# Kernel tuning notes

Measured on AMD Instinct MI355X. Metric: run time of the kernel, lower is better.

Reference implementation:

```python
import math
import jax, jax.numpy as jnp
import numpy as np

N, L, H, E, K = 4, 768, 8, 64, 1  # batch, seq (L==S), heads, feat, num_sines


def setup_inputs() -> dict:
    key = jax.random.key(0)
    ks = jax.random.split(key, 8)
    queries = jax.random.normal(ks[0], (N, L, H, E), jnp.float32)
    keys = jax.random.normal(ks[1], (N, L, H, E), jnp.float32)
    values = jax.random.normal(ks[2], (N, L, H, E), jnp.float32)
    attn_mask_add = jnp.zeros((L, L), jnp.float32)
    key_lengths_add = jnp.zeros((N, L), jnp.float32)
    freqs = jax.random.normal(ks[3], (H, E, K), jnp.float32) - 4.0  # init shift
    offsets = jax.random.normal(ks[4], (H, E, K), jnp.float32)
    gains = jax.random.normal(ks[5], (H, E, K), jnp.float32)
    # gains.data /= sqrt(||gains||_{-1}) / 2
    gains = gains / (jnp.sqrt(jnp.linalg.norm(gains, axis=-1, keepdims=True)) / 2.0)
    gate = jax.random.normal(ks[6], (H, E), jnp.float32)
    return dict(queries=queries, keys=keys, values=values,
                attn_mask_add=attn_mask_add, key_lengths_add=key_lengths_add,
                freqs=freqs, offsets=offsets, gains=gains, gate=gate)


def reference(queries, keys, values, attn_mask_add, key_lengths_add,
              freqs, offsets, gains, gate):
    n, l, h, e = queries.shape
    softmax_temp = 1.0 / math.sqrt(e)
    positions = jnp.arange(l, dtype=queries.dtype)  # (L,)
    f = jax.nn.sigmoid(freqs)[None] / 2.0  # (1,H,E,K)
    phases_q = 2.0 * math.pi * f * positions[:, None, None, None] + offsets[None]
    phases_k = 2.0 * math.pi * f * positions[:, None, None, None]
    # interleave cos/sin along last dim -> (L,H,E,2K)
    omega_q = jnp.stack([jnp.cos(phases_q), jnp.sin(phases_q)], axis=-1).reshape(l, h, e, 2 * f.shape[-1])
    omega_k = jnp.stack([jnp.cos(phases_k), jnp.sin(phases_k)], axis=-1).reshape(l, h, e, 2 * f.shape[-1])
    g = jax.nn.softplus(gains)
    g2 = jnp.stack([g, g], axis=-1).reshape(h, e, 2 * f.shape[-1])  # (H,E,2K)
    # positional kernel P: (L,S,H,E)
    P = jnp.einsum('lhdk,hdk,shdk->lshd', omega_q, g2 ** 2, omega_k)
    P = (1.0 - gate) * P + gate  # gated
    QK = jnp.einsum('nlhd,lshd,nshd->nhls', queries, P, keys)
    QK = QK + attn_mask_add[None, None] + key_lengths_add[:, None, None, :]
    A = jax.nn.softmax(softmax_temp * QK, axis=-1)
    V = jnp.einsum('nhls,nshd->nlhd', A, values)
    return V
```

## Files before the change

kernel.cpp:

```cpp
#include <hip/hip_runtime.h>
#include <math.h>
#include <stdint.h>

#define NB 4
#define LQ 768
#define NH 8
#define NE 64
#define ND 192
#define TEMP 0.125f

typedef _Float16 f16;
typedef __attribute__((ext_vector_type(8))) _Float16 f16x8;
typedef __attribute__((ext_vector_type(4))) float f32x4;

__device__ __forceinline__ void stage16(f16* lds_base, const f16* g, int lane) {
#if __has_builtin(__builtin_amdgcn_global_load_lds)
    __builtin_amdgcn_global_load_lds(
        (const __attribute__((address_space(1))) uint32_t*)g,
        (__attribute__((address_space(3))) uint32_t*)lds_base, 16, 0, 0);
#else
    *(uint4*)((char*)lds_base + lane * 16) = *(const uint4*)g;
#endif
}

__global__ __launch_bounds__(256) void sinattn_prep(
    const float* __restrict__ Q, const float* __restrict__ K,
    const float* __restrict__ freqs, const float* __restrict__ offsets,
    const float* __restrict__ gains, const float* __restrict__ gate,
    f16* __restrict__ Qf, f16* __restrict__ Kf)
{
    int idx = blockIdx.x * 256 + threadIdx.x;
    int eg = idx & 7, e0 = eg << 3;
    int h  = (idx >> 3) & 7;
    int t  = idx >> 6;
    int l  = t % LQ;
    int n  = t / LQ;
    int nh = (n << 3) | h;
    int he = (h << 6) | e0;

    const float* qp = Q + (size_t)idx * 8;
    const float* kp = K + (size_t)idx * 8;
    float4 q0 = *(const float4*)qp, q1 = *(const float4*)(qp + 4);
    float4 k0 = *(const float4*)kp, k1 = *(const float4*)(kp + 4);
    float qv[8] = {q0.x,q0.y,q0.z,q0.w, q1.x,q1.y,q1.z,q1.w};
    float kv[8] = {k0.x,k0.y,k0.z,k0.w, k1.x,k1.y,k1.z,k1.w};

    float4 fA = *(const float4*)(freqs   + he), fB = *(const float4*)(freqs   + he + 4);
    float4 oA = *(const float4*)(offsets + he), oB = *(const float4*)(offsets + he + 4);
    float4 gA = *(const float4*)(gains   + he), gB = *(const float4*)(gains   + he + 4);
    float4 tA = *(const float4*)(gate    + he), tB = *(const float4*)(gate    + he + 4);
    float fv[8] = {fA.x,fA.y,fA.z,fA.w, fB.x,fB.y,fB.z,fB.w};
    float ov[8] = {oA.x,oA.y,oA.z,oA.w, oB.x,oB.y,oB.z,oB.w};
    float gv[8] = {gA.x,gA.y,gA.z,gA.w, gB.x,gB.y,gB.z,gB.w};
    float tv[8] = {tA.x,tA.y,tA.z,tA.w, tB.x,tB.y,tB.z,tB.w};

    f16x8 oq0, oq1, oq2, ok0, ok1, ok2;
    float lf = (float)l;
    #pragma unroll
    for (int j = 0; j < 8; ++j) {
        float f  = 0.5f / (1.0f + __expf(-fv[j]));
        float gn = gv[j];
        float sp = (gn > 15.0f) ? gn : __logf(1.0f + __expf(gn));
        float gt = tv[j];
        float a  = (1.0f - gt) * sp * sp;
        float fh = __uint_as_float(__float_as_uint(f) & 0xFFFFF000u);
        float fl = f - fh;
        float t0 = lf * fh;
        float tr = t0 - floorf(t0);
        tr = __builtin_fmaf(lf, fl, tr);
        float pk = 6.28318530717958647f * tr;
        float pq = pk + ov[j];
        float sq = __sinf(pq), cq = __cosf(pq);
        float sk = __sinf(pk), ck = __cosf(pk);
        oq0[j] = (f16)(qv[j] * a * cq);
        oq1[j] = (f16)(qv[j] * a * sq);
        oq2[j] = (f16)(qv[j] * gt);
        ok0[j] = (f16)(kv[j] * ck);
        ok1[j] = (f16)(kv[j] * sk);
        ok2[j] = (f16)(kv[j]);
    }
    size_t base = ((size_t)nh * LQ + l) * ND + e0;
    *(f16x8*)(Qf + base)            = oq0;
    *(f16x8*)(Qf + base + NE)       = oq1;
    *(f16x8*)(Qf + base + 2 * NE)   = oq2;
    *(f16x8*)(Kf + base)            = ok0;
    *(f16x8*)(Kf + base + NE)       = ok1;
    *(f16x8*)(Kf + base + 2 * NE)   = ok2;
}

__global__ __launch_bounds__(256) void sinattn_vt(
    const float* __restrict__ V, f16* __restrict__ Vt)
{
    __shared__ f16 tile[64][72];
    int b = blockIdx.x;
    int st = b % 12, nh = b / 12;
    int n = nh >> 3, h = nh & 7;
    int s0 = st * 64;
    int tid = threadIdx.x;

    int sl = tid >> 2, e0 = (tid & 3) << 4;
    const float4* vp = (const float4*)(V + ((size_t)(n * LQ + s0 + sl) * NH + h) * NE + e0);
    float4 a0 = vp[0], a1 = vp[1], a2 = vp[2], a3 = vp[3];
    float vv[16] = { a0.x,a0.y,a0.z,a0.w, a1.x,a1.y,a1.z,a1.w,
                     a2.x,a2.y,a2.z,a2.w, a3.x,a3.y,a3.z,a3.w };
    #pragma unroll
    for (int j = 0; j < 16; ++j) tile[e0 + j][sl] = (f16)vv[j];
    __syncthreads();

    int er = tid >> 2, sc = tid & 3;
    f16* op = Vt + ((size_t)nh * NE + er) * LQ + s0 + sc * 16;
    *(uint4*)op       = *(const uint4*)&tile[er][sc * 16];
    *(uint4*)(op + 8) = *(const uint4*)&tile[er][sc * 16 + 8];
}

__global__ __launch_bounds__(256, 2) void sinattn_flash(
    const f16* __restrict__ Qf, const f16* __restrict__ Kf, const f16* __restrict__ Vt,
    const float* __restrict__ mask, const float* __restrict__ keylen,
    float* __restrict__ out)
{
    __shared__ __attribute__((aligned(16))) f16 sK[2][64 * 24 * 8];
    __shared__ __attribute__((aligned(16))) f16 sV[2][64 * 8 * 8];
    __shared__ __attribute__((aligned(16))) f16 sP[4][16 * 72];

    int tid  = threadIdx.x;
    int wv   = tid >> 6;
    int lane = tid & 63;
    int grp  = lane >> 4;
    int r16  = lane & 15;
    int swz  = r16 & 7;

    int bid = blockIdx.x;
    int nh  = bid & 31;
    int lt  = bid >> 5;
    int n   = nh >> 3;
    int l0  = lt * 64;

    f16x8 qf[6];
    {
        size_t rbase = ((size_t)nh * LQ + l0 + wv * 16 + r16) * ND + grp * 8;
        #pragma unroll
        for (int d0 = 0; d0 < 6; ++d0)
            qf[d0] = *(const f16x8*)(Qf + rbase + d0 * 32);
    }

    int goffK[6], goffV[2];
    #pragma unroll
    for (int i = 0; i < 6; ++i) {
        int p = i * 256 + wv * 64 + lane;
        int r = p / 24, c = p - r * 24;
        int cl = (c & ~7) | ((c & 7) ^ (r & 7));
        goffK[i] = r * ND + cl * 8;
    }
    #pragma unroll
    for (int i = 0; i < 2; ++i) {
        int p = i * 256 + wv * 64 + lane;
        int r = p >> 3, c = p & 7;
        goffV[i] = r * LQ + (c ^ (r & 7)) * 8;
    }
    const f16* Kb = Kf + (size_t)nh * LQ * ND;
    const f16* Vb = Vt + (size_t)nh * NE * LQ;

    {
        #pragma unroll
        for (int i = 0; i < 6; ++i)
            stage16(&sK[0][(i * 256 + wv * 64) * 8], Kb + goffK[i], lane);
        #pragma unroll
        for (int i = 0; i < 2; ++i)
            stage16(&sV[0][(i * 256 + wv * 64) * 8], Vb + goffV[i], lane);
    }

    float m_i[4], l_i[4];
    f32x4 O[4];
    #pragma unroll
    for (int rr = 0; rr < 4; ++rr) { m_i[rr] = -INFINITY; l_i[rr] = 0.f; }
    #pragma unroll
    for (int tt = 0; tt < 4; ++tt)
        #pragma unroll
        for (int rr = 0; rr < 4; ++rr) O[tt][rr] = 0.f;

    for (int c = 0; c < 12; ++c) {
        int cur = c & 1;
        int s0  = c * 64;
        __syncthreads();

        if (c < 11) {
            const f16* kg = Kb + (s0 + 64) * ND;
            const f16* vg = Vb + (s0 + 64);
            #pragma unroll
            for (int i = 0; i < 6; ++i)
                stage16(&sK[cur ^ 1][(i * 256 + wv * 64) * 8], kg + goffK[i], lane);
            #pragma unroll
            for (int i = 0; i < 2; ++i)
                stage16(&sV[cur ^ 1][(i * 256 + wv * 64) * 8], vg + goffV[i], lane);
        }

        float klv[4], mreg[4][4];
        #pragma unroll
        for (int j = 0; j < 4; ++j) klv[j] = keylen[n * LQ + s0 + j * 16 + r16];
        #pragma unroll
        for (int rr = 0; rr < 4; ++rr) {
            int lrow = l0 + wv * 16 + grp * 4 + rr;
            #pragma unroll
            for (int j = 0; j < 4; ++j)
                mreg[rr][j] = mask[lrow * LQ + s0 + j * 16 + r16];
        }

        f32x4 st[4];
        #pragma unroll
        for (int j = 0; j < 4; ++j)
            #pragma unroll
            for (int rr = 0; rr < 4; ++rr) st[j][rr] = 0.f;
        #pragma unroll
        for (int d0 = 0; d0 < 6; ++d0) {
            #pragma unroll
            for (int j = 0; j < 4; ++j) {
                int cc = d0 * 4 + grp;
                int cl = (cc & ~7) | ((cc & 7) ^ swz);
                f16x8 bf = *(const f16x8*)&sK[cur][((j * 16 + r16) * 24 + cl) * 8];
                st[j] = __builtin_amdgcn_mfma_f32_16x16x32_f16(qf[d0], bf, st[j], 0, 0, 0);
            }
        }

        #pragma unroll
        for (int rr = 0; rr < 4; ++rr) {
            float lg[4];
            float mx = -INFINITY;
            #pragma unroll
            for (int j = 0; j < 4; ++j) {
                lg[j] = TEMP * (st[j][rr] + mreg[rr][j] + klv[j]);
                mx = fmaxf(mx, lg[j]);
            }
            #pragma unroll
            for (int d = 1; d < 16; d <<= 1) mx = fmaxf(mx, __shfl_xor(mx, d));
            float mnew  = fmaxf(m_i[rr], mx);
            float alpha = __expf(m_i[rr] - mnew);
            float rs = 0.f;
            #pragma unroll
            for (int j = 0; j < 4; ++j) {
                float p = __expf(lg[j] - mnew);
                rs += p;
                sP[wv][(grp * 4 + rr) * 72 + j * 16 + r16] = (f16)p;
            }
            #pragma unroll
            for (int d = 1; d < 16; d <<= 1) rs += __shfl_xor(rs, d);
            l_i[rr] = l_i[rr] * alpha + rs;
            m_i[rr] = mnew;
            #pragma unroll
            for (int tt = 0; tt < 4; ++tt) O[tt][rr] *= alpha;
        }

        #pragma unroll
        for (int kk = 0; kk < 2; ++kk) {
            f16x8 pa = *(const f16x8*)&sP[wv][r16 * 72 + kk * 32 + grp * 8];
            #pragma unroll
            for (int tt = 0; tt < 4; ++tt) {
                int cc = kk * 4 + grp;
                f16x8 vb = *(const f16x8*)&sV[cur][((tt * 16 + r16) * 8 + (cc ^ swz)) * 8];
                O[tt] = __builtin_amdgcn_mfma_f32_16x16x32_f16(pa, vb, O[tt], 0, 0, 0);
            }
        }
    }

    #pragma unroll
    for (int rr = 0; rr < 4; ++rr) {
        float inv = 1.0f / l_i[rr];
        int lrow = l0 + wv * 16 + grp * 4 + rr;
        float* op = out + ((size_t)(n * LQ + lrow) * NH + (nh & 7)) * NE;
        #pragma unroll
        for (int tt = 0; tt < 4; ++tt)
            op[tt * 16 + r16] = O[tt][rr] * inv;
    }
}

extern "C" void kernel_launch(void* const* d_in, const int* in_sizes, int n_in,
                              void* d_out, int out_size, void* d_ws, size_t ws_size,
                              hipStream_t stream)
{
    const float* Q      = (const float*)d_in[0];
    const float* K      = (const float*)d_in[1];
    const float* V      = (const float*)d_in[2];
    const float* mask   = (const float*)d_in[3];
    const float* keylen = (const float*)d_in[4];
    const float* freqs  = (const float*)d_in[5];
    const float* offs   = (const float*)d_in[6];
    const float* gains  = (const float*)d_in[7];
    const float* gate   = (const float*)d_in[8];
    float* out = (float*)d_out;

    const size_t P = (size_t)NB * NH * LQ * ND;
    f16* Qf = (f16*)d_ws;
    f16* Kf = Qf + P;
    f16* Vt = Kf + P;

    sinattn_prep<<<768, 256, 0, stream>>>(Q, K, freqs, offs, gains, gate, Qf, Kf);
    sinattn_vt<<<384, 256, 0, stream>>>(V, Vt);
    sinattn_flash<<<NB * NH * (LQ / 64), 256, 0, stream>>>(Qf, Kf, Vt,
                                                           mask, keylen, out);
}
```

Baseline: 121.6 us.

## Load K and V MFMA operands directly from global memory instead of LDS

Removes the double-buffered LDS staging of K and V tiles and the per-chunk block barrier. Each wave now reads its MFMA B operands straight from global memory, relying on L2/L1 to serve the data shared among the four waves of a block. It also raises wave priority around the MFMA sections with s_setprio. The risk is redundant global traffic, since each wave now fetches the full K/V chunk separately, and exposed load latency with no explicit prefetch.

New measurement: 183.7 us. +51.1%, slower.

```diff
diff --git a/kernel.cpp b/kernel.cpp
--- a/kernel.cpp
+++ b/kernel.cpp
@@ -12,16 +12,6 @@
 typedef _Float16 f16;
 typedef __attribute__((ext_vector_type(8))) _Float16 f16x8;
 typedef __attribute__((ext_vector_type(4))) float f32x4;
-
-__device__ __forceinline__ void stage16(f16* lds_base, const f16* g, int lane) {
-#if __has_builtin(__builtin_amdgcn_global_load_lds)
-    __builtin_amdgcn_global_load_lds(
-        (const __attribute__((address_space(1))) uint32_t*)g,
-        (__attribute__((address_space(3))) uint32_t*)lds_base, 16, 0, 0);
-#else
-    *(uint4*)((char*)lds_base + lane * 16) = *(const uint4*)g;
-#endif
-}
 
 __global__ __launch_bounds__(256) void sinattn_prep(
     const float* __restrict__ Q, const float* __restrict__ K,
@@ -118,8 +108,6 @@
     const float* __restrict__ mask, const float* __restrict__ keylen,
     float* __restrict__ out)
 {
-    __shared__ __attribute__((aligned(16))) f16 sK[2][64 * 24 * 8];
-    __shared__ __attribute__((aligned(16))) f16 sV[2][64 * 8 * 8];
     __shared__ __attribute__((aligned(16))) f16 sP[4][16 * 72];
 
     int tid  = threadIdx.x;
@@ -127,7 +115,6 @@
     int lane = tid & 63;
     int grp  = lane >> 4;
     int r16  = lane & 15;
-    int swz  = r16 & 7;
 
     int bid = blockIdx.x;
     int nh  = bid & 31;
@@ -143,31 +130,8 @@
             qf[d0] = *(const f16x8*)(Qf + rbase + d0 * 32);
     }
 
-    int goffK[6], goffV[2];
-    #pragma unroll
-    for (int i = 0; i < 6; ++i) {
-        int p = i * 256 + wv * 64 + lane;
-        int r = p / 24, c = p - r * 24;
-        int cl = (c & ~7) | ((c & 7) ^ (r & 7));
-        goffK[i] = r * ND + cl * 8;
-    }
-    #pragma unroll
-    for (int i = 0; i < 2; ++i) {
-        int p = i * 256 + wv * 64 + lane;
-        int r = p >> 3, c = p & 7;
-        goffV[i] = r * LQ + (c ^ (r & 7)) * 8;
-    }
-    const f16* Kb = Kf + (size_t)nh * LQ * ND;
-    const f16* Vb = Vt + (size_t)nh * NE * LQ;
-
-    {
-        #pragma unroll
-        for (int i = 0; i < 6; ++i)
-            stage16(&sK[0][(i * 256 + wv * 64) * 8], Kb + goffK[i], lane);
-        #pragma unroll
-        for (int i = 0; i < 2; ++i)
-            stage16(&sV[0][(i * 256 + wv * 64) * 8], Vb + goffV[i], lane);
-    }
+    const f16* Kb = Kf + (size_t)nh * LQ * ND + (size_t)r16 * ND + grp * 8;
+    const f16* Vb = Vt + ((size_t)nh * NE + r16) * LQ + grp * 8;
 
     float m_i[4], l_i[4];
     f32x4 O[4];
@@ -179,20 +143,7 @@
         for (int rr = 0; rr < 4; ++rr) O[tt][rr] = 0.f;
 
     for (int c = 0; c < 12; ++c) {
-        int cur = c & 1;
-        int s0  = c * 64;
-        __syncthreads();
-
-        if (c < 11) {
-            const f16* kg = Kb + (s0 + 64) * ND;
-            const f16* vg = Vb + (s0 + 64);
-            #pragma unroll
-            for (int i = 0; i < 6; ++i)
-                stage16(&sK[cur ^ 1][(i * 256 + wv * 64) * 8], kg + goffK[i], lane);
-            #pragma unroll
-            for (int i = 0; i < 2; ++i)
-                stage16(&sV[cur ^ 1][(i * 256 + wv * 64) * 8], vg + goffV[i], lane);
-        }
+        int s0 = c * 64;
 
         float klv[4], mreg[4][4];
         #pragma unroll
@@ -210,16 +161,16 @@
         for (int j = 0; j < 4; ++j)
             #pragma unroll
             for (int rr = 0; rr < 4; ++rr) st[j][rr] = 0.f;
+        __builtin_amdgcn_s_setprio(1);
         #pragma unroll
         for (int d0 = 0; d0 < 6; ++d0) {
             #pragma unroll
             for (int j = 0; j < 4; ++j) {
-                int cc = d0 * 4 + grp;
-                int cl = (cc & ~7) | ((cc & 7) ^ swz);
-                f16x8 bf = *(const f16x8*)&sK[cur][((j * 16 + r16) * 24 + cl) * 8];
+                f16x8 bf = *(const f16x8*)(Kb + (size_t)(s0 + j * 16) * ND + d0 * 32);
                 st[j] = __builtin_amdgcn_mfma_f32_16x16x32_f16(qf[d0], bf, st[j], 0, 0, 0);
             }
         }
+        __builtin_amdgcn_s_setprio(0);
 
         #pragma unroll
         for (int rr = 0; rr < 4; ++rr) {
@@ -249,16 +200,17 @@
             for (int tt = 0; tt < 4; ++tt) O[tt][rr] *= alpha;
         }
 
+        __builtin_amdgcn_s_setprio(1);
         #pragma unroll
         for (int kk = 0; kk < 2; ++kk) {
             f16x8 pa = *(const f16x8*)&sP[wv][r16 * 72 + kk * 32 + grp * 8];
             #pragma unroll
             for (int tt = 0; tt < 4; ++tt) {
-                int cc = kk * 4 + grp;
-                f16x8 vb = *(const f16x8*)&sV[cur][((tt * 16 + r16) * 8 + (cc ^ swz)) * 8];
+                f16x8 vb = *(const f16x8*)(Vb + (size_t)(tt * 16) * LQ + s0 + kk * 32);
                 O[tt] = __builtin_amdgcn_mfma_f32_16x16x32_f16(pa, vb, O[tt], 0, 0, 0);
             }
         }
+        __builtin_amdgcn_s_setprio(0);
     }
 
     #pragma unroll
```

## Use two waves per block each computing 32 query rows, DPP row reductions

Applied to the files above, without the earlier changes.

The flash kernel drops from four waves of 16 query rows to two waves of 32 rows, so each K/V fragment read from LDS feeds two MFMAs, halving LDS B-operand traffic per FLOP. Each thread now issues twice as many async global->LDS loads to fill the tiles. Softmax row max/sum reductions switch from __shfl_xor to DPP row operations to avoid LDS-backed shuffles. The cost is more registers per thread and fewer waves per block (128 threads) to hide latency.

Result: no change. 122.4 us (+0.7%).

```diff
diff --git a/kernel.cpp b/kernel.cpp
--- a/kernel.cpp
+++ b/kernel.cpp
@@ -21,6 +21,28 @@
 #else
     *(uint4*)((char*)lds_base + lane * 16) = *(const uint4*)g;
 #endif
+}
+
+template <int CTRL>
+__device__ __forceinline__ float dppf(float x) {
+    union { float f; int i; } u, r;
+    u.f = x;
+    r.i = __builtin_amdgcn_update_dpp(u.i, u.i, CTRL, 0xF, 0xF, false);
+    return r.f;
+}
+__device__ __forceinline__ float red16_max(float x) {
+    x = fmaxf(x, dppf<0xB1>(x));
+    x = fmaxf(x, dppf<0x4E>(x));
+    x = fmaxf(x, dppf<0x141>(x));
+    x = fmaxf(x, dppf<0x140>(x));
+    return x;
+}
+__device__ __forceinline__ float red16_sum(float x) {
+    x += dppf<0xB1>(x);
+    x += dppf<0x4E>(x);
+    x += dppf<0x141>(x);
+    x += dppf<0x140>(x);
+    return x;
 }
 
 __global__ __launch_bounds__(256) void sinattn_prep(
@@ -113,14 +135,14 @@
     *(uint4*)(op + 8) = *(const uint4*)&tile[er][sc * 16 + 8];
 }
 
-__global__ __launch_bounds__(256, 2) void sinattn_flash(
+__global__ __launch_bounds__(128, 2) void sinattn_flash(
     const f16* __restrict__ Qf, const f16* __restrict__ Kf, const f16* __restrict__ Vt,
     const float* __restrict__ mask, const float* __restrict__ keylen,
     float* __restrict__ out)
 {
     __shared__ __attribute__((aligned(16))) f16 sK[2][64 * 24 * 8];
     __shared__ __attribute__((aligned(16))) f16 sV[2][64 * 8 * 8];
-    __shared__ __attribute__((aligned(16))) f16 sP[4][16 * 72];
+    __shared__ __attribute__((aligned(16))) f16 sP[2][32 * 72];
 
     int tid  = threadIdx.x;
     int wv   = tid >> 6;
@@ -135,25 +157,26 @@
     int n   = nh >> 3;
     int l0  = lt * 64;
 
-    f16x8 qf[6];
-    {
-        size_t rbase = ((size_t)nh * LQ + l0 + wv * 16 + r16) * ND + grp * 8;
+    f16x8 qf[2][6];
+    #pragma unroll
+    for (int ti = 0; ti < 2; ++ti) {
+        size_t rbase = ((size_t)nh * LQ + l0 + wv * 32 + ti * 16 + r16) * ND + grp * 8;
         #pragma unroll
         for (int d0 = 0; d0 < 6; ++d0)
-            qf[d0] = *(const f16x8*)(Qf + rbase + d0 * 32);
-    }
-
-    int goffK[6], goffV[2];
-    #pragma unroll
-    for (int i = 0; i < 6; ++i) {
-        int p = i * 256 + wv * 64 + lane;
+            qf[ti][d0] = *(const f16x8*)(Qf + rbase + d0 * 32);
+    }
+
+    int goffK[12], goffV[4];
+    #pragma unroll
+    for (int i = 0; i < 12; ++i) {
+        int p = i * 128 + tid;
         int r = p / 24, c = p - r * 24;
         int cl = (c & ~7) | ((c & 7) ^ (r & 7));
         goffK[i] = r * ND + cl * 8;
     }
     #pragma unroll
-    for (int i = 0; i < 2; ++i) {
-        int p = i * 256 + wv * 64 + lane;
+    for (int i = 0; i < 4; ++i) {
+        int p = i * 128 + tid;
         int r = p >> 3, c = p & 7;
         goffV[i] = r * LQ + (c ^ (r & 7)) * 8;
     }
@@ -162,21 +185,25 @@
 
     {
         #pragma unroll
-        for (int i = 0; i < 6; ++i)
-            stage16(&sK[0][(i * 256 + wv * 64) * 8], Kb + goffK[i], lane);
-        #pragma unroll
-        for (int i = 0; i < 2; ++i)
-            stage16(&sV[0][(i * 256 + wv * 64) * 8], Vb + goffV[i], lane);
-    }
-
-    float m_i[4], l_i[4];
-    f32x4 O[4];
-    #pragma unroll
-    for (int rr = 0; rr < 4; ++rr) { m_i[rr] = -INFINITY; l_i[rr] = 0.f; }
-    #pragma unroll
-    for (int tt = 0; tt < 4; ++tt)
-        #pragma unroll
-        for (int rr = 0; rr < 4; ++rr) O[tt][rr] = 0.f;
+        for (int i = 0; i < 12; ++i)
+            stage16(&sK[0][(i * 128 + wv * 64) * 8], Kb + goffK[i], lane);
+        #pragma unroll
+        for (int i = 0; i < 4; ++i)
+            stage16(&sV[0][(i * 128 + wv * 64) * 8], Vb + goffV[i], lane);
+    }
+
+    float m_i[2][4], l_i[2][4];
+    f32x4 O[2][4];
+    #pragma unroll
+    for (int ti = 0; ti < 2; ++ti)
+        #pragma unroll
+        for (int rr = 0; rr < 4; ++rr) { m_i[ti][rr] = -INFINITY; l_i[ti][rr] = 0.f; }
+    #pragma unroll
+    for (int ti = 0; ti < 2; ++ti)
+        #pragma unroll
+        for (int tt = 0; tt < 4; ++tt)
+            #pragma unroll
+            for (int rr = 0; rr < 4; ++rr) O[ti][tt][rr] = 0.f;
 
     for (int c = 0; c < 12; ++c) {
         int cur = c & 1;
@@ -187,29 +214,33 @@
             const f16* kg = Kb + (s0 + 64) * ND;
             const f16* vg = Vb + (s0 + 64);
             #pragma unroll
-            for (int i = 0; i < 6; ++i)
-                stage16(&sK[cur ^ 1][(i * 256 + wv * 64) * 8], kg + goffK[i], lane);
-            #pragma unroll
-            for (int i = 0; i < 2; ++i)
-                stage16(&sV[cur ^ 1][(i * 256 + wv * 64) * 8], vg + goffV[i], lane);
-        }
-
-        float klv[4], mreg[4][4];
+            for (int i = 0; i < 12; ++i)
+                stage16(&sK[cur ^ 1][(i * 128 + wv * 64) * 8], kg + goffK[i], lane);
+            #pragma unroll
+            for (int i = 0; i < 4; ++i)
+                stage16(&sV[cur ^ 1][(i * 128 + wv * 64) * 8], vg + goffV[i], lane);
+        }
+
+        float klv[4], mreg[2][4][4];
         #pragma unroll
         for (int j = 0; j < 4; ++j) klv[j] = keylen[n * LQ + s0 + j * 16 + r16];
         #pragma unroll
-        for (int rr = 0; rr < 4; ++rr) {
-            int lrow = l0 + wv * 16 + grp * 4 + rr;
+        for (int ti = 0; ti < 2; ++ti)
+            #pragma unroll
+            for (int rr = 0; rr < 4; ++rr) {
+                int lrow = l0 + wv * 32 + ti * 16 + grp * 4 + rr;
+                #pragma unroll
+                for (int j = 0; j < 4; ++j)
+                    mreg[ti][rr][j] = mask[lrow * LQ + s0 + j * 16 + r16];
+            }
+
+        f32x4 st[2][4];
+        #pragma unroll
+        for (int ti = 0; ti < 2; ++ti)
             #pragma unroll
             for (int j = 0; j < 4; ++j)
-                mreg[rr][j] = mask[lrow * LQ + s0 + j * 16 + r16];
-        }
-
-        f32x4 st[4];
-        #pragma unroll
-        for (int j = 0; j < 4; ++j)
-            #pragma unroll
-            for (int rr = 0; rr < 4; ++rr) st[j][rr] = 0.f;
+                #pragma unroll
+                for (int rr = 0; rr < 4; ++rr) st[ti][j][rr] = 0.f;
         #pragma unroll
         for (int d0 = 0; d0 < 6; ++d0) {
             #pragma unroll
@@ -217,58 +248,65 @@
                 int cc = d0 * 4 + grp;
                 int cl = (cc & ~7) | ((cc & 7) ^ swz);
                 f16x8 bf = *(const f16x8*)&sK[cur][((j * 16 + r16) * 24 + cl) * 8];
-                st[j] = __builtin_amdgcn_mfma_f32_16x16x32_f16(qf[d0], bf, st[j], 0, 0, 0);
+                st[0][j] = __builtin_amdgcn_mfma_f32_16x16x32_f16(qf[0][d0], bf, st[0][j], 0, 0, 0);
+                st[1][j] = __builtin_amdgcn_mfma_f32_16x16x32_f16(qf[1][d0], bf, st[1][j], 0, 0, 0);
             }
         }
 
         #pragma unroll
-        for (int rr = 0; rr < 4; ++rr) {
-            float lg[4];
-            float mx = -INFINITY;
-            #pragma unroll
-            for (int j = 0; j < 4; ++j) {
-                lg[j] = TEMP * (st[j][rr] + mreg[rr][j] + klv[j]);
-                mx = fmaxf(mx, lg[j]);
+        for (int ti = 0; ti < 2; ++ti) {
+            #pragma unroll
+            for (int rr = 0; rr < 4; ++rr) {
+                float lg[4];
+                float mx = -INFINITY;
+                #pragma unroll
+                for (int j = 0; j < 4; ++j) {
+                    lg[j] = TEMP * (st[ti][j][rr] + mreg[ti][rr][j] + klv[j]);
+                    mx = fmaxf(mx, lg[j]);
+                }
+                mx = red16_max(mx);
+                float mnew  = fmaxf(m_i[ti][rr], mx);
+                float alpha = __expf(m_i[ti][rr] - mnew);
+                float rs = 0.f;
+                #pragma unroll
+                for (int j = 0; j < 4; ++j) {
+                    float p = __expf(lg[j] - mnew);
+                    rs += p;
+                    sP[wv][(ti * 16 + grp * 4 + rr) * 72 + j * 16 + r16] = (f16)p;
+                }
+                rs = red16_sum(rs);
+                l_i[ti][rr] = l_i[ti][rr] * alpha + rs;
+                m_i[ti][rr] = mnew;
+                #pragma unroll
+                for (int tt = 0; tt < 4; ++tt) O[ti][tt][rr] *= alpha;
             }
-            #pragma unroll
-            for (int d = 1; d < 16; d <<= 1) mx = fmaxf(mx, __shfl_xor(mx, d));
-            float mnew  = fmaxf(m_i[rr], mx);
-            float alpha = __expf(m_i[rr] - mnew);
-            float rs = 0.f;
-            #pragma unroll
-            for (int j = 0; j < 4; ++j) {
-                float p = __expf(lg[j] - mnew);
-                rs += p;
-                sP[wv][(grp * 4 + rr) * 72 + j * 16 + r16] = (f16)p;
-            }
-            #pragma unroll
-            for (int d = 1; d < 16; d <<= 1) rs += __shfl_xor(rs, d);
-            l_i[rr] = l_i[rr] * alpha + rs;
-            m_i[rr] = mnew;
-            #pragma unroll
-            for (int tt = 0; tt < 4; ++tt) O[tt][rr] *= alpha;
         }
 
         #pragma unroll
         for (int kk = 0; kk < 2; ++kk) {
-            f16x8 pa = *(const f16x8*)&sP[wv][r16 * 72 + kk * 32 + grp * 8];
+            f16x8 pa0 = *(const f16x8*)&sP[wv][(r16) * 72 + kk * 32 + grp * 8];
+            f16x8 pa1 = *(const f16x8*)&sP[wv][(16 + r16) * 72 + kk * 32 + grp * 8];
             #pragma unroll
             for (int tt = 0; tt < 4; ++tt) {
                 int cc = kk * 4 + grp;
                 f16x8 vb = *(const f16x8*)&sV[cur][((tt * 16 + r16) * 8 + (cc ^ swz)) * 8];
-                O[tt] = __builtin_amdgcn_mfma_f32_16x16x32_f16(pa, vb, O[tt], 0, 0, 0);
+                O[0][tt] = __builtin_amdgcn_mfma_f32_16x16x32_f16(pa0, vb, O[0][tt], 0, 0, 0);
+                O[1][tt] = __builtin_amdgcn_mfma_f32_16x16x32_f16(pa1, vb, O[1][tt], 0, 0, 0);
             }
         }
     }
 
     #pragma unroll
-    for (int rr = 0; rr < 4; ++rr) {
-        float inv = 1.0f / l_i[rr];
-        int lrow = l0 + wv * 16 + grp * 4 + rr;
-        float* op = out + ((size_t)(n * LQ + lrow) * NH + (nh & 7)) * NE;
-        #pragma unroll
-        for (int tt = 0; tt < 4; ++tt)
-            op[tt * 16 + r16] = O[tt][rr] * inv;
+    for (int ti = 0; ti < 2; ++ti) {
+        #pragma unroll
+        for (int rr = 0; rr < 4; ++rr) {
+            float inv = 1.0f / l_i[ti][rr];
+            int lrow = l0 + wv * 32 + ti * 16 + grp * 4 + rr;
+            float* op = out + ((size_t)(n * LQ + lrow) * NH + (nh & 7)) * NE;
+            #pragma unroll
+            for (int tt = 0; tt < 4; ++tt)
+                op[tt * 16 + r16] = O[ti][tt][rr] * inv;
+        }
     }
 }
 
@@ -294,6 +332,6 @@
 
     sinattn_prep<<<768, 256, 0, stream>>>(Q, K, freqs, offs, gains, gate, Qf, Kf);
     sinattn_vt<<<384, 256, 0, stream>>>(V, Vt);
-    sinattn_flash<<<NB * NH * (LQ / 64), 256, 0, stream>>>(Qf, Kf, Vt,
+    sinattn_flash<<<NB * NH * (LQ / 64), 128, 0, stream>>>(Qf, Kf, Vt,
                                                            mask, keylen, out);
 }
```

## Use 48-row query tiles with 3 waves, exp2 softmax and DPP row reductions

Applied to the files above, without the earlier changes.

The flash kernel now processes 48 query rows per block with 3 waves, raising the grid from 384 to 512 blocks so the 256-CU GPU is better filled. The K/V staging loops are redistributed over 192 threads. Softmax switches to base-2 exponentials with a pre-scaled temperature, and row max/sum reductions use DPP instead of shfl_xor. The trade-off is more redundant K/V loading per query row, and the DPP row_shr patterns need to match the earlier xor-reduction semantics across 16 lanes.

Result: faster. 116.9 us (-3.9%).

```diff
diff --git a/kernel.cpp b/kernel.cpp
--- a/kernel.cpp
+++ b/kernel.cpp
@@ -7,7 +7,7 @@
 #define NH 8
 #define NE 64
 #define ND 192
-#define TEMP 0.125f
+#define TEMP2 0.18033688011112042f
 
 typedef _Float16 f16;
 typedef __attribute__((ext_vector_type(8))) _Float16 f16x8;
@@ -21,6 +21,36 @@
 #else
     *(uint4*)((char*)lds_base + lane * 16) = *(const uint4*)g;
 #endif
+}
+
+__device__ __forceinline__ float fexp2(float x) {
+#if __has_builtin(__builtin_amdgcn_exp2f)
+    return __builtin_amdgcn_exp2f(x);
+#else
+    return exp2f(x);
+#endif
+}
+
+template <int CTRL>
+__device__ __forceinline__ float dppf(float x) {
+    union { float f; int i; } u, r;
+    u.f = x;
+    r.i = __builtin_amdgcn_update_dpp(u.i, u.i, CTRL, 0xF, 0xF, false);
+    return r.f;
+}
+__device__ __forceinline__ float red16_max(float x) {
+    x = fmaxf(x, dppf<0xB1>(x));
+    x = fmaxf(x, dppf<0x4E>(x));
+    x = fmaxf(x, dppf<0x141>(x));
+    x = fmaxf(x, dppf<0x140>(x));
+    return x;
+}
+__device__ __forceinline__ float red16_sum(float x) {
+    x += dppf<0xB1>(x);
+    x += dppf<0x4E>(x);
+    x += dppf<0x141>(x);
+    x += dppf<0x140>(x);
+    return x;
 }
 
 __global__ __launch_bounds__(256) void sinattn_prep(
@@ -113,17 +143,17 @@
     *(uint4*)(op + 8) = *(const uint4*)&tile[er][sc * 16 + 8];
 }
 
-__global__ __launch_bounds__(256, 2) void sinattn_flash(
+__global__ __launch_bounds__(192) void sinattn_flash(
     const f16* __restrict__ Qf, const f16* __restrict__ Kf, const f16* __restrict__ Vt,
     const float* __restrict__ mask, const float* __restrict__ keylen,
     float* __restrict__ out)
 {
     __shared__ __attribute__((aligned(16))) f16 sK[2][64 * 24 * 8];
     __shared__ __attribute__((aligned(16))) f16 sV[2][64 * 8 * 8];
-    __shared__ __attribute__((aligned(16))) f16 sP[4][16 * 72];
+    __shared__ __attribute__((aligned(16))) f16 sP[3][16 * 72];
 
     int tid  = threadIdx.x;
-    int wv   = tid >> 6;
+    int wv   = tid / 64;
     int lane = tid & 63;
     int grp  = lane >> 4;
     int r16  = lane & 15;
@@ -133,27 +163,20 @@
     int nh  = bid & 31;
     int lt  = bid >> 5;
     int n   = nh >> 3;
-    int l0  = lt * 64;
-
-    f16x8 qf[6];
-    {
-        size_t rbase = ((size_t)nh * LQ + l0 + wv * 16 + r16) * ND + grp * 8;
-        #pragma unroll
-        for (int d0 = 0; d0 < 6; ++d0)
-            qf[d0] = *(const f16x8*)(Qf + rbase + d0 * 32);
-    }
-
-    int goffK[6], goffV[2];
-    #pragma unroll
-    for (int i = 0; i < 6; ++i) {
-        int p = i * 256 + wv * 64 + lane;
+    int l0  = lt * 48;
+    int qrow0 = l0 + wv * 16;
+
+    int goffK[8], goffV[3];
+    #pragma unroll
+    for (int i = 0; i < 8; ++i) {
+        int p = i * 192 + tid;
         int r = p / 24, c = p - r * 24;
         int cl = (c & ~7) | ((c & 7) ^ (r & 7));
         goffK[i] = r * ND + cl * 8;
     }
     #pragma unroll
-    for (int i = 0; i < 2; ++i) {
-        int p = i * 256 + wv * 64 + lane;
+    for (int i = 0; i < 3; ++i) {
+        int p = i * 192 + tid;
         int r = p >> 3, c = p & 7;
         goffV[i] = r * LQ + (c ^ (r & 7)) * 8;
     }
@@ -162,11 +185,21 @@
 
     {
         #pragma unroll
-        for (int i = 0; i < 6; ++i)
-            stage16(&sK[0][(i * 256 + wv * 64) * 8], Kb + goffK[i], lane);
+        for (int i = 0; i < 8; ++i)
+            stage16(&sK[0][(i * 192 + wv * 64) * 8], Kb + goffK[i], lane);
         #pragma unroll
         for (int i = 0; i < 2; ++i)
-            stage16(&sV[0][(i * 256 + wv * 64) * 8], Vb + goffV[i], lane);
+            stage16(&sV[0][(i * 192 + wv * 64) * 8], Vb + goffV[i], lane);
+        if (tid < 128)
+            stage16(&sV[0][(384 + wv * 64) * 8], Vb + goffV[2], lane);
+    }
+
+    f16x8 qf[6];
+    {
+        size_t rbase = ((size_t)nh * LQ + qrow0 + r16) * ND + grp * 8;
+        #pragma unroll
+        for (int d0 = 0; d0 < 6; ++d0)
+            qf[d0] = *(const f16x8*)(Qf + rbase + d0 * 32);
     }
 
     float m_i[4], l_i[4];
@@ -187,11 +220,13 @@
             const f16* kg = Kb + (s0 + 64) * ND;
             const f16* vg = Vb + (s0 + 64);
             #pragma unroll
-            for (int i = 0; i < 6; ++i)
-                stage16(&sK[cur ^ 1][(i * 256 + wv * 64) * 8], kg + goffK[i], lane);
+            for (int i = 0; i < 8; ++i)
+                stage16(&sK[cur ^ 1][(i * 192 + wv * 64) * 8], kg + goffK[i], lane);
             #pragma unroll
             for (int i = 0; i < 2; ++i)
-                stage16(&sV[cur ^ 1][(i * 256 + wv * 64) * 8], vg + goffV[i], lane);
+                stage16(&sV[cur ^ 1][(i * 192 + wv * 64) * 8], vg + goffV[i], lane);
+            if (tid < 128)
+                stage16(&sV[cur ^ 1][(384 + wv * 64) * 8], vg + goffV[2], lane);
         }
 
         float klv[4], mreg[4][4];
@@ -199,7 +234,7 @@
         for (int j = 0; j < 4; ++j) klv[j] = keylen[n * LQ + s0 + j * 16 + r16];
         #pragma unroll
         for (int rr = 0; rr < 4; ++rr) {
-            int lrow = l0 + wv * 16 + grp * 4 + rr;
+            int lrow = qrow0 + grp * 4 + rr;
             #pragma unroll
             for (int j = 0; j < 4; ++j)
                 mreg[rr][j] = mask[lrow * LQ + s0 + j * 16 + r16];
@@ -227,22 +262,20 @@
             float mx = -INFINITY;
             #pragma unroll
             for (int j = 0; j < 4; ++j) {
-                lg[j] = TEMP * (st[j][rr] + mreg[rr][j] + klv[j]);
+                lg[j] = TEMP2 * (st[j][rr] + mreg[rr][j] + klv[j]);
                 mx = fmaxf(mx, lg[j]);
             }
-            #pragma unroll
-            for (int d = 1; d < 16; d <<= 1) mx = fmaxf(mx, __shfl_xor(mx, d));
+            mx = red16_max(mx);
             float mnew  = fmaxf(m_i[rr], mx);
-            float alpha = __expf(m_i[rr] - mnew);
+            float alpha = fexp2(m_i[rr] - mnew);
             float rs = 0.f;
             #pragma unroll
             for (int j = 0; j < 4; ++j) {
-                float p = __expf(lg[j] - mnew);
+                float p = fexp2(lg[j] - mnew);
                 rs += p;
                 sP[wv][(grp * 4 + rr) * 72 + j * 16 + r16] = (f16)p;
             }
-            #pragma unroll
-            for (int d = 1; d < 16; d <<= 1) rs += __shfl_xor(rs, d);
+            rs = red16_sum(rs);
             l_i[rr] = l_i[rr] * alpha + rs;
             m_i[rr] = mnew;
             #pragma unroll
@@ -264,7 +297,7 @@
     #pragma unroll
     for (int rr = 0; rr < 4; ++rr) {
         float inv = 1.0f / l_i[rr];
-        int lrow = l0 + wv * 16 + grp * 4 + rr;
+        int lrow = qrow0 + grp * 4 + rr;
         float* op = out + ((size_t)(n * LQ + lrow) * NH + (nh & 7)) * NE;
         #pragma unroll
         for (int tt = 0; tt < 4; ++tt)
@@ -294,6 +327,6 @@
 
     sinattn_prep<<<768, 256, 0, stream>>>(Q, K, freqs, offs, gains, gate, Qf, Kf);
     sinattn_vt<<<384, 256, 0, stream>>>(V, Vt);
-    sinattn_flash<<<NB * NH * (LQ / 64), 256, 0, stream>>>(Qf, Kf, Vt,
+    sinattn_flash<<<NB * NH * (LQ / 48), 192, 0, stream>>>(Qf, Kf, Vt,
                                                            mask, keylen, out);
 }
```
